# Optimization experiments

Measured on AMD Instinct MI355X. Metric: run time of the kernel, lower is better.

The kernel has to match this reference:

```python
import jax, jax.numpy as jnp
import numpy as np

N_NODES = 100000
N_EDGES = 1600000
HIDDEN_DIM = 64
EIGS_DIM = 32


def setup_inputs() -> dict:
    key = jax.random.key(0)
    k1, k2, k3, k4, k5 = jax.random.split(key, 5)
    q = jax.random.normal(k1, (N_NODES, HIDDEN_DIM), dtype=jnp.float32)
    k = jax.random.normal(k2, (N_NODES, HIDDEN_DIM), dtype=jnp.float32)
    v = jax.random.normal(k3, (N_NODES, HIDDEN_DIM), dtype=jnp.float32)
    eigs = jax.random.normal(k4, (N_NODES, EIGS_DIM), dtype=jnp.float32)
    lambda0 = jnp.zeros((1,), dtype=jnp.float32)  # nn.Parameter(torch.zeros(1))
    indices = jax.random.randint(k5, (2, N_EDGES), 0, N_NODES, dtype=jnp.int64)
    return {"q": q, "k": k, "v": v, "eigs": eigs, "lambda0": lambda0,
            "indices": indices}


def reference(q, k, v, eigs, lambda0, indices):
    n = q.shape[0]
    inv_sqrt_dim = 1.0 / jnp.sqrt(jnp.asarray(q.shape[1], dtype=q.dtype))
    i0 = indices[0]  # destination/row node per edge
    i1 = indices[1]  # source/col node per edge

    # per-edge attention logits: gather-dot-product
    x = jnp.sum(q[i0] * k[i1], axis=-1) * inv_sqrt_dim          # [E]
    y = jnp.sum(eigs[i0] * eigs[i1], axis=-1)                   # [E]
    s = x + jnp.exp(lambda0[0]) * y                             # [E]

    # sparse softmax: clamp(exp(s), -5, 5) then segment-normalize by row sum
    e = jnp.clip(jnp.exp(s), -5.0, 5.0)                         # [E]
    denom = jax.ops.segment_sum(e, i0, num_segments=n)          # [N]
    denom = jnp.where(denom == 0.0, 1.0, denom)
    w = e / denom[i0]                                           # [E]

    # spmm: out[r] = sum_{edges with row r} w_e * v[col_e]
    out = jax.ops.segment_sum(w[:, None] * v[i1], i0, num_segments=n)  # [N, D]
    return out
```

## Files before the change

kernel.cpp:

```cpp
#include <hip/hip_runtime.h>
#include <hip/hip_fp16.h>


#define HD 64
#define ED 32
#define CAP 64
#define RPP 256
#define PSHIFT 8
#define D1 36
#define NB1 256
#define PCAP 5120
#define SPILL_CAP 131072

struct h4 { __half2 a, b; };

__global__ void cvt16_kernel(const float* __restrict__ src,
                             __half* __restrict__ dst, long long n4) {
    long long t = (long long)blockIdx.x * blockDim.x + threadIdx.x;
    long long stride = (long long)gridDim.x * blockDim.x;
    for (; t < n4; t += stride) {
        float4 f = ((const float4*)src)[t];
        h4 h;
        h.a = __floats2half2_rn(f.x, f.y);
        h.b = __floats2half2_rn(f.z, f.w);
        ((h4*)dst)[t] = h;
    }
}

__global__ void p1_bin_kernel(const int* __restrict__ idx, int n_edges,
                              int NP, int chunk,
                              int* __restrict__ part, int* __restrict__ gcur,
                              long long* __restrict__ spill,
                              int* __restrict__ spill_cnt,
                              int* __restrict__ flag) {
    extern __shared__ int sm[];
    int* cnt   = sm;
    int* sbase = sm + NP;
    int* bins  = sm + 2 * NP;
    int tid = threadIdx.x;

    for (int i = tid; i < NP; i += 256) cnt[i] = 0;
    __syncthreads();

    int e0 = blockIdx.x * chunk;
    int n  = n_edges - e0; if (n > chunk) n = chunk; if (n < 0) n = 0;

    for (int i = tid; i < n; i += 256) {
        int e = e0 + i;
        int r = idx[e];
        int c = idx[n_edges + e];
        int p = r >> PSHIFT;
        int w = ((r & (RPP - 1)) << 17) | c;
        int pos = atomicAdd(&cnt[p], 1);
        if (pos < D1) {
            bins[p * D1 + pos] = w;
        } else {
            int s = atomicAdd(spill_cnt, 1);
            if (s < SPILL_CAP) spill[s] = ((long long)r << 32) | (unsigned)c;
            else *flag = 1;
        }
    }
    __syncthreads();

    for (int p = tid; p < NP; p += 256) {
        int m = cnt[p]; if (m > D1) m = D1;
        sbase[p] = (m > 0) ? atomicAdd(&gcur[p], m) : 0;
    }
    __syncthreads();

    int wave = tid >> 6;
    int lane = tid & 63;
    for (int p = wave; p < NP; p += 4) {
        int m = cnt[p]; if (m > D1) m = D1;
        if (lane < m) {
            int slot = sbase[p] + lane;
            int w = bins[p * D1 + lane];
            if (slot < PCAP) {
                part[p * PCAP + slot] = w;
            } else {
                int r = (p << PSHIFT) | (w >> 17);
                int c = w & 0x1FFFF;
                int s = atomicAdd(spill_cnt, 1);
                if (s < SPILL_CAP) spill[s] = ((long long)r << 32) | (unsigned)c;
                else *flag = 1;
            }
        }
    }
}

__global__ void p2_bucket_kernel(const int* __restrict__ part,
                                 const int* __restrict__ gcur,
                                 int* __restrict__ count,
                                 int* __restrict__ bucket, int n_nodes) {
    __shared__ int cnt[RPP / 2];
    __shared__ int win[(RPP / 2) * CAP];
    int tid = threadIdx.x;
    if (tid < RPP / 2) cnt[tid] = 0;
    __syncthreads();

    int p    = blockIdx.x >> 1;
    int half = blockIdx.x & 1;
    int n = gcur[p]; if (n > PCAP) n = PCAP;

    for (int i = tid; i < n; i += 256) {
        int w  = part[p * PCAP + i];
        int rl = w >> 17;
        if ((rl >> 7) != half) continue;
        int rh = rl & 127;
        int c  = w & 0x1FFFF;
        int pos = atomicAdd(&cnt[rh], 1);
        if (pos < CAP) win[(rh << 6) + pos] = c;
    }
    __syncthreads();

    int r0 = (p << PSHIFT) + (half << 7);
    int rows = n_nodes - r0;
    if (rows > RPP / 2) rows = RPP / 2;
    if (rows > 0) {
        int nint4 = rows * (CAP / 4);
        int4* dst = (int4*)(bucket + (long long)r0 * CAP);
        const int4* src = (const int4*)win;
        for (int i = tid; i < nint4; i += 256) dst[i] = src[i];
        if (tid < rows) count[r0 + tid] = cnt[tid];
    }
}

__global__ void spill_drain_kernel(const long long* __restrict__ spill,
                                   const int* __restrict__ spill_cnt,
                                   int* __restrict__ count,
                                   int* __restrict__ bucket) {
    int ns = *spill_cnt; if (ns > SPILL_CAP) ns = SPILL_CAP;
    int stride = gridDim.x * blockDim.x;
    for (int t = blockIdx.x * blockDim.x + threadIdx.x; t < ns; t += stride) {
        long long wc = spill[t];
        int r = (int)(wc >> 32);
        int c = (int)(wc & 0xFFFFFFFFLL);
        int pos = atomicAdd(&count[r], 1);
        if (pos < CAP) bucket[(long long)r * CAP + pos] = c;
    }
}

__global__ void repair_zero_kernel(const int* __restrict__ flag,
                                   int* __restrict__ count, int n_nodes) {
    if (*flag == 0) return;
    int t = blockIdx.x * blockDim.x + threadIdx.x;
    if (t < n_nodes) count[t] = 0;
}

__global__ void repair_scatter_kernel(const int* __restrict__ flag,
                                      const int* __restrict__ idx,
                                      int* __restrict__ count,
                                      int* __restrict__ bucket, int n_edges) {
    if (*flag == 0) return;
    int t = blockIdx.x * blockDim.x + threadIdx.x;
    if (t < n_edges) {
        int r = idx[t];
        int c = idx[n_edges + t];
        int p = atomicAdd(&count[r], 1);
        if (p < CAP) bucket[(long long)r * CAP + p] = c;
    }
}

__global__ void bucket_scatter_kernel(const int* __restrict__ idx,
                                      int* __restrict__ count,
                                      int* __restrict__ bucket, int n_edges) {
    int t = blockIdx.x * blockDim.x + threadIdx.x;
    if (t < n_edges) {
        int r = idx[t];
        int c = idx[n_edges + t];
        int p = atomicAdd(&count[r], 1);
        if (p < CAP) bucket[(long long)r * CAP + p] = c;
    }
}

__global__ void row16_kernel(const float* __restrict__ q,
                             const __half* __restrict__ k16,
                             const __half* __restrict__ v16,
                             const float* __restrict__ eigs,
                             const __half* __restrict__ e16,
                             const float* __restrict__ lambda0,
                             const int* __restrict__ counts,
                             const int* __restrict__ col,
                             const float* __restrict__ kf,
                             const float* __restrict__ vf,
                             const int* __restrict__ idx, int n_edges,
                             float* __restrict__ out, int n_nodes) {
    long long tid = (long long)blockIdx.x * blockDim.x + threadIdx.x;
    int r = (int)(tid >> 6);
    if (r >= n_nodes) return;
    int lane = threadIdx.x & 63;
    int sub = lane & 15;
    int grp = lane >> 4;

    int deg = counts[r];
    const float expL = __expf(lambda0[0]);

    if (deg > CAP) {
        float qs = q[(long long)r * HD + lane] * 0.125f;
        float gs = (lane < ED) ? eigs[(long long)r * ED + lane] * expL : 0.f;
        float accs = 0.f, den = 0.f;
        for (int base = 0; base < n_edges; base += 64) {
            int e = base + lane;
            int rr = (e < n_edges) ? idx[e] : -1;
            int cc = (e < n_edges) ? idx[n_edges + e] : 0;
            unsigned long long mm = __ballot(rr == r);
            while (mm) {
                int b = __ffsll(mm) - 1;
                mm &= mm - 1;
                int c = __shfl(cc, b, 64);
                float kb = kf[(long long)c * HD + lane];
                float gb = (lane < ED) ? eigs[(long long)c * ED + lane] : 0.f;
                float s = qs * kb + gs * gb;
                #pragma unroll
                for (int off = 32; off > 0; off >>= 1) s += __shfl_xor(s, off, 64);
                float e1 = fminf(__expf(s), 5.0f);
                den += e1;
                accs += e1 * vf[(long long)c * HD + lane];
            }
        }
        float inv = (den == 0.f) ? 1.f : __frcp_rn(den);
        out[(long long)r * HD + lane] = accs * inv;
        return;
    }

    long long start = (long long)r * CAP;

    float4 qa = *(const float4*)(q    + (long long)r * HD + sub * 4);
    float2 ga = *(const float2*)(eigs + (long long)r * ED + sub * 2);
    qa.x *= 0.125f; qa.y *= 0.125f; qa.z *= 0.125f; qa.w *= 0.125f;
    ga.x *= expL;   ga.y *= expL;

    float4 acc = make_float4(0.f, 0.f, 0.f, 0.f);
    float den = 0.f;

    for (int base = 0; base < deg; base += 64) {
        int m = deg - base; if (m > 64) m = 64;
        int cl = (lane < m) ? col[start + base + lane] : 0;
        for (int j = 0; j < m; j += 16) {
            int c1 = __shfl(cl, j + grp,      64);
            int c2 = __shfl(cl, j + 4 + grp,  64);
            int c3 = __shfl(cl, j + 8 + grp,  64);
            int c4 = __shfl(cl, j + 12 + grp, 64);
            h4 kb1 = *(const h4*)(k16 + (long long)c1 * HD + sub * 4);
            __half2 gh1 = *(const __half2*)(e16 + (long long)c1 * ED + sub * 2);
            h4 vv1 = *(const h4*)(v16 + (long long)c1 * HD + sub * 4);
            h4 kb2 = *(const h4*)(k16 + (long long)c2 * HD + sub * 4);
            __half2 gh2 = *(const __half2*)(e16 + (long long)c2 * ED + sub * 2);
            h4 vv2 = *(const h4*)(v16 + (long long)c2 * HD + sub * 4);
            h4 kb3 = *(const h4*)(k16 + (long long)c3 * HD + sub * 4);
            __half2 gh3 = *(const __half2*)(e16 + (long long)c3 * ED + sub * 2);
            h4 vv3 = *(const h4*)(v16 + (long long)c3 * HD + sub * 4);
            h4 kb4 = *(const h4*)(k16 + (long long)c4 * HD + sub * 4);
            __half2 gh4 = *(const __half2*)(e16 + (long long)c4 * ED + sub * 2);
            h4 vv4 = *(const h4*)(v16 + (long long)c4 * HD + sub * 4);

            float s1 = qa.x*__low2float(kb1.a) + qa.y*__high2float(kb1.a)
                     + qa.z*__low2float(kb1.b) + qa.w*__high2float(kb1.b)
                     + ga.x*__low2float(gh1)   + ga.y*__high2float(gh1);
            float s2 = qa.x*__low2float(kb2.a) + qa.y*__high2float(kb2.a)
                     + qa.z*__low2float(kb2.b) + qa.w*__high2float(kb2.b)
                     + ga.x*__low2float(gh2)   + ga.y*__high2float(gh2);
            float s3 = qa.x*__low2float(kb3.a) + qa.y*__high2float(kb3.a)
                     + qa.z*__low2float(kb3.b) + qa.w*__high2float(kb3.b)
                     + ga.x*__low2float(gh3)   + ga.y*__high2float(gh3);
            float s4 = qa.x*__low2float(kb4.a) + qa.y*__high2float(kb4.a)
                     + qa.z*__low2float(kb4.b) + qa.w*__high2float(kb4.b)
                     + ga.x*__low2float(gh4)   + ga.y*__high2float(gh4);
            #pragma unroll
            for (int off = 8; off > 0; off >>= 1) {
                s1 += __shfl_xor(s1, off, 64);
                s2 += __shfl_xor(s2, off, 64);
                s3 += __shfl_xor(s3, off, 64);
                s4 += __shfl_xor(s4, off, 64);
            }
            float e1 = fminf(__expf(s1), 5.0f);
            float e2 = fminf(__expf(s2), 5.0f);
            float e3 = fminf(__expf(s3), 5.0f);
            float e4 = fminf(__expf(s4), 5.0f);

            if (j + grp < m) {
                den += e1;
                acc.x += e1 * __low2float(vv1.a); acc.y += e1 * __high2float(vv1.a);
                acc.z += e1 * __low2float(vv1.b); acc.w += e1 * __high2float(vv1.b);
            }
            if (j + 4 + grp < m) {
                den += e2;
                acc.x += e2 * __low2float(vv2.a); acc.y += e2 * __high2float(vv2.a);
                acc.z += e2 * __low2float(vv2.b); acc.w += e2 * __high2float(vv2.b);
            }
            if (j + 8 + grp < m) {
                den += e3;
                acc.x += e3 * __low2float(vv3.a); acc.y += e3 * __high2float(vv3.a);
                acc.z += e3 * __low2float(vv3.b); acc.w += e3 * __high2float(vv3.b);
            }
            if (j + 12 + grp < m) {
                den += e4;
                acc.x += e4 * __low2float(vv4.a); acc.y += e4 * __high2float(vv4.a);
                acc.z += e4 * __low2float(vv4.b); acc.w += e4 * __high2float(vv4.b);
            }
        }
    }

    #pragma unroll
    for (int off = 16; off < 64; off <<= 1) {
        acc.x += __shfl_xor(acc.x, off, 64);
        acc.y += __shfl_xor(acc.y, off, 64);
        acc.z += __shfl_xor(acc.z, off, 64);
        acc.w += __shfl_xor(acc.w, off, 64);
        den   += __shfl_xor(den,   off, 64);
    }

    if (grp == 0) {
        float inv = (den == 0.0f) ? 1.0f : __frcp_rn(den);
        float4 o = make_float4(acc.x * inv, acc.y * inv, acc.z * inv, acc.w * inv);
        *(float4*)(out + (long long)r * HD + sub * 4) = o;
    }
}

__global__ void row_kernel(const float* __restrict__ q, const float* __restrict__ k,
                           const float* __restrict__ v, const float* __restrict__ eigs,
                           const float* __restrict__ lambda0,
                           const int* __restrict__ counts,
                           const int* __restrict__ col,
                           const int* __restrict__ idx, int n_edges,
                           float* __restrict__ out, int n_nodes) {
    long long tid = (long long)blockIdx.x * blockDim.x + threadIdx.x;
    int r = (int)(tid >> 6);
    if (r >= n_nodes) return;
    int lane = threadIdx.x & 63;
    int sub = lane & 15;
    int grp = lane >> 4;

    int deg = counts[r];
    const float expL = __expf(lambda0[0]);

    if (deg > CAP) {
        float qs = q[(long long)r * HD + lane] * 0.125f;
        float gs = (lane < ED) ? eigs[(long long)r * ED + lane] * expL : 0.f;
        float accs = 0.f, den = 0.f;
        for (int base = 0; base < n_edges; base += 64) {
            int e = base + lane;
            int rr = (e < n_edges) ? idx[e] : -1;
            int cc = (e < n_edges) ? idx[n_edges + e] : 0;
            unsigned long long mm = __ballot(rr == r);
            while (mm) {
                int b = __ffsll(mm) - 1;
                mm &= mm - 1;
                int c = __shfl(cc, b, 64);
                float kb = k[(long long)c * HD + lane];
                float gb = (lane < ED) ? eigs[(long long)c * ED + lane] : 0.f;
                float s = qs * kb + gs * gb;
                #pragma unroll
                for (int off = 32; off > 0; off >>= 1) s += __shfl_xor(s, off, 64);
                float e1 = fminf(__expf(s), 5.0f);
                den += e1;
                accs += e1 * v[(long long)c * HD + lane];
            }
        }
        float inv = (den == 0.f) ? 1.f : __frcp_rn(den);
        out[(long long)r * HD + lane] = accs * inv;
        return;
    }

    long long start = (long long)r * CAP;

    float4 qa = *(const float4*)(q    + (long long)r * HD + sub * 4);
    float2 ga = *(const float2*)(eigs + (long long)r * ED + sub * 2);
    qa.x *= 0.125f; qa.y *= 0.125f; qa.z *= 0.125f; qa.w *= 0.125f;
    ga.x *= expL;   ga.y *= expL;

    float4 acc = make_float4(0.f, 0.f, 0.f, 0.f);
    float den = 0.f;

    for (int base = 0; base < deg; base += 64) {
        int m = deg - base; if (m > 64) m = 64;
        int cl = (lane < m) ? col[start + base + lane] : 0;
        for (int j = 0; j < m; j += 8) {
            int c1 = __shfl(cl, j + grp,     64);
            int c2 = __shfl(cl, j + 4 + grp, 64);
            float4 kb1 = *(const float4*)(k    + (long long)c1 * HD + sub * 4);
            float2 gb1 = *(const float2*)(eigs + (long long)c1 * ED + sub * 2);
            float4 vv1 = *(const float4*)(v    + (long long)c1 * HD + sub * 4);
            float4 kb2 = *(const float4*)(k    + (long long)c2 * HD + sub * 4);
            float2 gb2 = *(const float2*)(eigs + (long long)c2 * ED + sub * 2);
            float4 vv2 = *(const float4*)(v    + (long long)c2 * HD + sub * 4);

            float s1 = qa.x*kb1.x + qa.y*kb1.y + qa.z*kb1.z + qa.w*kb1.w
                     + ga.x*gb1.x + ga.y*gb1.y;
            float s2 = qa.x*kb2.x + qa.y*kb2.y + qa.z*kb2.z + qa.w*kb2.w
                     + ga.x*gb2.x + ga.y*gb2.y;
            #pragma unroll
            for (int off = 8; off > 0; off >>= 1) {
                s1 += __shfl_xor(s1, off, 64);
                s2 += __shfl_xor(s2, off, 64);
            }
            float e1 = fminf(__expf(s1), 5.0f);
            float e2 = fminf(__expf(s2), 5.0f);

            if (j + grp < m) {
                den += e1;
                acc.x += e1 * vv1.x; acc.y += e1 * vv1.y;
                acc.z += e1 * vv1.z; acc.w += e1 * vv1.w;
            }
            if (j + 4 + grp < m) {
                den += e2;
                acc.x += e2 * vv2.x; acc.y += e2 * vv2.y;
                acc.z += e2 * vv2.z; acc.w += e2 * vv2.w;
            }
        }
    }

    #pragma unroll
    for (int off = 16; off < 64; off <<= 1) {
        acc.x += __shfl_xor(acc.x, off, 64);
        acc.y += __shfl_xor(acc.y, off, 64);
        acc.z += __shfl_xor(acc.z, off, 64);
        acc.w += __shfl_xor(acc.w, off, 64);
        den   += __shfl_xor(den,   off, 64);
    }

    if (grp == 0) {
        float inv = (den == 0.0f) ? 1.0f : __frcp_rn(den);
        float4 o = make_float4(acc.x * inv, acc.y * inv, acc.z * inv, acc.w * inv);
        *(float4*)(out + (long long)r * HD + sub * 4) = o;
    }
}

__global__ void edge_fused_kernel(const float* __restrict__ q,
                                  const float* __restrict__ k,
                                  const float* __restrict__ v,
                                  const float* __restrict__ eigs,
                                  const float* __restrict__ lambda0,
                                  const int* __restrict__ idx,
                                  float* __restrict__ denom,
                                  float* __restrict__ out, int n_edges) {
    long long gid = (long long)blockIdx.x * blockDim.x + threadIdx.x;
    int lane = threadIdx.x & 63;
    int edge = (int)(gid >> 4);
    int sub  = (int)(gid & 15);
    int valid = (edge < n_edges);
    int ec = valid ? edge : (n_edges - 1);
    int i0 = idx[ec];
    int i1 = idx[n_edges + ec];
    const float expL = __expf(lambda0[0]);
    float4 qa = *(const float4*)(q + (long long)i0 * HD + sub * 4);
    float4 kb = *(const float4*)(k + (long long)i1 * HD + sub * 4);
    float c = (qa.x*kb.x + qa.y*kb.y + qa.z*kb.z + qa.w*kb.w) * 0.125f;
    float2 ea = *(const float2*)(eigs + (long long)i0 * ED + sub * 2);
    float2 eb = *(const float2*)(eigs + (long long)i1 * ED + sub * 2);
    c += expL * (ea.x * eb.x + ea.y * eb.y);
    #pragma unroll
    for (int off = 8; off > 0; off >>= 1) c += __shfl_xor(c, off, 64);
    float e = fminf(__expf(c), 5.0f);
    if (valid && sub == 0) atomicAdd(&denom[i0], e);
    #pragma unroll
    for (int j = 0; j < 4; ++j) {
        float ej = __shfl(e,     j * 16, 64);
        int   r  = __shfl(i0,    j * 16, 64);
        int   s  = __shfl(i1,    j * 16, 64);
        int   vj = __shfl(valid, j * 16, 64);
        if (vj) {
            float vv = v[(long long)s * HD + lane];
            atomicAdd(&out[(long long)r * HD + lane], ej * vv);
        }
    }
}

__global__ void normalize_kernel(float* __restrict__ out,
                                 const float* __restrict__ denom, int n_nodes) {
    int t = blockIdx.x * blockDim.x + threadIdx.x;
    int total = n_nodes * (HD / 4);
    if (t >= total) return;
    int row = t >> 4;
    float d = denom[row];
    float inv = (d == 0.0f) ? 1.0f : __frcp_rn(d);
    float4* o4 = (float4*)out;
    float4 x = o4[t];
    x.x *= inv; x.y *= inv; x.z *= inv; x.w *= inv;
    o4[t] = x;
}

extern "C" void kernel_launch(void* const* d_in, const int* in_sizes, int n_in,
                              void* d_out, int out_size, void* d_ws, size_t ws_size,
                              hipStream_t stream) {
    const float* q       = (const float*)d_in[0];
    const float* k       = (const float*)d_in[1];
    const float* v       = (const float*)d_in[2];
    const float* eigs    = (const float*)d_in[3];
    const float* lambda0 = (const float*)d_in[4];
    const int*   idx     = (const int*)d_in[5];

    const int n_edges = in_sizes[5] / 2;
    const int n_nodes = in_sizes[0] / HD;

    const int NP = (n_nodes + RPP - 1) / RPP;
    const int eb = (n_edges + 255) / 256;
    long long rthreads = (long long)n_nodes * 64;
    const int rb = (int)((rthreads + 255) / 256);

    size_t ints1 = ((size_t)n_nodes + (size_t)n_nodes * CAP
                    + (size_t)NP * PCAP + NP + 2) * sizeof(int);
    size_t need1  = ints1 + 8 + (size_t)SPILL_CAP * sizeof(long long);
    size_t h16    = (size_t)n_nodes * (HD + HD + ED) * sizeof(__half);
    size_t need16 = h16 + need1;
    size_t need2  = ((size_t)n_nodes + (size_t)n_nodes * CAP) * sizeof(int);

    if (ws_size >= need16) {
        char* base = (char*)d_ws;
        __half* k16 = (__half*)base;
        __half* v16 = k16 + (size_t)n_nodes * HD;
        __half* e16 = v16 + (size_t)n_nodes * HD;
        int* count     = (int*)(e16 + (size_t)n_nodes * ED);
        int* bucket    = count + n_nodes;
        int* part      = bucket + (size_t)n_nodes * CAP;
        int* gcur      = part + (size_t)NP * PCAP;
        int* spill_cnt = gcur + NP;
        int* flag      = spill_cnt + 1;
        size_t soff = (size_t)((char*)(flag + 1) - base);
        soff = (soff + 7) & ~(size_t)7;
        long long* spill = (long long*)(base + soff);

        hipMemsetAsync(gcur, 0, (size_t)(NP + 2) * sizeof(int), stream);

        cvt16_kernel<<<1024, 256, 0, stream>>>(k, k16, (long long)n_nodes * HD / 4);
        cvt16_kernel<<<1024, 256, 0, stream>>>(v, v16, (long long)n_nodes * HD / 4);
        cvt16_kernel<<<1024, 256, 0, stream>>>(eigs, e16, (long long)n_nodes * ED / 4);

        int chunk = (n_edges + NB1 - 1) / NB1;
        size_t smbytes = (size_t)NP * (2 + D1) * sizeof(int);
        p1_bin_kernel<<<NB1, 256, smbytes, stream>>>(idx, n_edges, NP, chunk,
                                                     part, gcur, spill,
                                                     spill_cnt, flag);
        p2_bucket_kernel<<<2 * NP, 256, 0, stream>>>(part, gcur, count, bucket,
                                                     n_nodes);
        spill_drain_kernel<<<256, 256, 0, stream>>>(spill, spill_cnt, count,
                                                    bucket);
        repair_zero_kernel<<<(n_nodes + 255) / 256, 256, 0, stream>>>(flag, count,
                                                                      n_nodes);
        repair_scatter_kernel<<<eb, 256, 0, stream>>>(flag, idx, count, bucket,
                                                      n_edges);
        row16_kernel<<<rb, 256, 0, stream>>>(q, k16, v16, eigs, e16, lambda0,
                                             count, bucket, k, v, idx, n_edges,
                                             (float*)d_out, n_nodes);
    } else if (ws_size >= need1) {
        char* base = (char*)d_ws;
        int* count     = (int*)base;
        int* bucket    = count + n_nodes;
        int* part      = bucket + (size_t)n_nodes * CAP;
        int* gcur      = part + (size_t)NP * PCAP;
        int* spill_cnt = gcur + NP;
        int* flag      = spill_cnt + 1;
        size_t soff = (size_t)((char*)(flag + 1) - base);
        soff = (soff + 7) & ~(size_t)7;
        long long* spill = (long long*)(base + soff);

        hipMemsetAsync(gcur, 0, (size_t)(NP + 2) * sizeof(int), stream);

        int chunk = (n_edges + NB1 - 1) / NB1;
        size_t smbytes = (size_t)NP * (2 + D1) * sizeof(int);
        p1_bin_kernel<<<NB1, 256, smbytes, stream>>>(idx, n_edges, NP, chunk,
                                                     part, gcur, spill,
                                                     spill_cnt, flag);
        p2_bucket_kernel<<<2 * NP, 256, 0, stream>>>(part, gcur, count, bucket,
                                                     n_nodes);
        spill_drain_kernel<<<256, 256, 0, stream>>>(spill, spill_cnt, count,
                                                    bucket);
        repair_zero_kernel<<<(n_nodes + 255) / 256, 256, 0, stream>>>(flag, count,
                                                                      n_nodes);
        repair_scatter_kernel<<<eb, 256, 0, stream>>>(flag, idx, count, bucket,
                                                      n_edges);
        row_kernel<<<rb, 256, 0, stream>>>(q, k, v, eigs, lambda0, count, bucket,
                                           idx, n_edges, (float*)d_out, n_nodes);
    } else if (ws_size >= need2) {
        int* count  = (int*)d_ws;
        int* bucket = count + n_nodes;
        hipMemsetAsync(count, 0, (size_t)n_nodes * sizeof(int), stream);
        bucket_scatter_kernel<<<eb, 256, 0, stream>>>(idx, count, bucket, n_edges);
        row_kernel<<<rb, 256, 0, stream>>>(q, k, v, eigs, lambda0, count, bucket,
                                           idx, n_edges, (float*)d_out, n_nodes);
    } else {
        float* denom = (float*)d_ws;
        hipMemsetAsync(denom, 0, (size_t)n_nodes * sizeof(float), stream);
        hipMemsetAsync(d_out, 0, (size_t)out_size * sizeof(float), stream);
        long long threads = (long long)n_edges * 16;
        int grid = (int)((threads + 255) / 256);
        edge_fused_kernel<<<grid, 256, 0, stream>>>(q, k, v, eigs, lambda0, idx,
                                                    denom, (float*)d_out, n_edges);
        int n4 = n_nodes * (HD / 4);
        normalize_kernel<<<(n4 + 255) / 256, 256, 0, stream>>>((float*)d_out,
                                                               denom, n_nodes);
    }
}
```

Baseline: 276.3 us.

## Fuse fp16 conversion into binning kernel, merge spill/repair kernels, retune binning

The three separate fp32-to-fp16 conversion launches are folded into the tail of the edge-binning kernel, and the spill-drain and repair-zero kernels are merged into one launch. The binning kernel now runs 1024 blocks with a smaller per-partition shared bin depth of 16, and its flush loop handles four partitions per wave using 16-lane subgroups. This cuts launch count and raises parallelism in binning. The smaller bins push more edges onto the global spill path, so more atomics may hit the spill counter.

```diff
diff --git a/kernel.cpp b/kernel.cpp
--- a/kernel.cpp
+++ b/kernel.cpp
@@ -7,32 +7,26 @@
 #define CAP 64
 #define RPP 256
 #define PSHIFT 8
-#define D1 36
-#define NB1 256
+#define D1 16
+#define NB1 1024
 #define PCAP 5120
 #define SPILL_CAP 131072
 
 struct h4 { __half2 a, b; };
-
-__global__ void cvt16_kernel(const float* __restrict__ src,
-                             __half* __restrict__ dst, long long n4) {
-    long long t = (long long)blockIdx.x * blockDim.x + threadIdx.x;
-    long long stride = (long long)gridDim.x * blockDim.x;
-    for (; t < n4; t += stride) {
-        float4 f = ((const float4*)src)[t];
-        h4 h;
-        h.a = __floats2half2_rn(f.x, f.y);
-        h.b = __floats2half2_rn(f.z, f.w);
-        ((h4*)dst)[t] = h;
-    }
-}
 
 __global__ void p1_bin_kernel(const int* __restrict__ idx, int n_edges,
                               int NP, int chunk,
                               int* __restrict__ part, int* __restrict__ gcur,
                               long long* __restrict__ spill,
                               int* __restrict__ spill_cnt,
-                              int* __restrict__ flag) {
+                              int* __restrict__ flag,
+                              const float* __restrict__ kf,
+                              const float* __restrict__ vf,
+                              const float* __restrict__ ef,
+                              __half* __restrict__ k16,
+                              __half* __restrict__ v16,
+                              __half* __restrict__ e16,
+                              long long nk4, long long ne4) {
     extern __shared__ int sm[];
     int* cnt   = sm;
     int* sbase = sm + NP;
@@ -70,20 +64,51 @@
 
     int wave = tid >> 6;
     int lane = tid & 63;
-    for (int p = wave; p < NP; p += 4) {
-        int m = cnt[p]; if (m > D1) m = D1;
-        if (lane < m) {
-            int slot = sbase[p] + lane;
-            int w = bins[p * D1 + lane];
-            if (slot < PCAP) {
-                part[p * PCAP + slot] = w;
-            } else {
-                int r = (p << PSHIFT) | (w >> 17);
-                int c = w & 0x1FFFF;
-                int s = atomicAdd(spill_cnt, 1);
-                if (s < SPILL_CAP) spill[s] = ((long long)r << 32) | (unsigned)c;
-                else *flag = 1;
-            }
+    int sg = lane >> 4;
+    int sl = lane & 15;
+    for (int p0 = wave * 4; p0 < NP; p0 += 16) {
+        int p = p0 + sg;
+        if (p < NP) {
+            int m = cnt[p]; if (m > D1) m = D1;
+            if (sl < m) {
+                int slot = sbase[p] + sl;
+                int w = bins[p * D1 + sl];
+                if (slot < PCAP) {
+                    part[p * PCAP + slot] = w;
+                } else {
+                    int r = (p << PSHIFT) | (w >> 17);
+                    int c = w & 0x1FFFF;
+                    int s = atomicAdd(spill_cnt, 1);
+                    if (s < SPILL_CAP) spill[s] = ((long long)r << 32) | (unsigned)c;
+                    else *flag = 1;
+                }
+            }
+        }
+    }
+
+    if (k16 != nullptr) {
+        long long gt = (long long)blockIdx.x * 256 + tid;
+        long long gs = (long long)gridDim.x * 256;
+        for (long long t = gt; t < nk4; t += gs) {
+            float4 f = ((const float4*)kf)[t];
+            h4 h;
+            h.a = __floats2half2_rn(f.x, f.y);
+            h.b = __floats2half2_rn(f.z, f.w);
+            ((h4*)k16)[t] = h;
+        }
+        for (long long t = gt; t < nk4; t += gs) {
+            float4 f = ((const float4*)vf)[t];
+            h4 h;
+            h.a = __floats2half2_rn(f.x, f.y);
+            h.b = __floats2half2_rn(f.z, f.w);
+            ((h4*)v16)[t] = h;
+        }
+        for (long long t = gt; t < ne4; t += gs) {
+            float4 f = ((const float4*)ef)[t];
+            h4 h;
+            h.a = __floats2half2_rn(f.x, f.y);
+            h.b = __floats2half2_rn(f.z, f.w);
+            ((h4*)e16)[t] = h;
         }
     }
 }
@@ -125,26 +150,25 @@
     }
 }
 
-__global__ void spill_drain_kernel(const long long* __restrict__ spill,
-                                   const int* __restrict__ spill_cnt,
-                                   int* __restrict__ count,
-                                   int* __restrict__ bucket) {
+__global__ void spill_or_zero_kernel(const long long* __restrict__ spill,
+                                     const int* __restrict__ spill_cnt,
+                                     const int* __restrict__ flag,
+                                     int* __restrict__ count,
+                                     int* __restrict__ bucket, int n_nodes) {
+    int stride = gridDim.x * blockDim.x;
+    int t0 = blockIdx.x * blockDim.x + threadIdx.x;
+    if (*flag) {
+        for (int t = t0; t < n_nodes; t += stride) count[t] = 0;
+        return;
+    }
     int ns = *spill_cnt; if (ns > SPILL_CAP) ns = SPILL_CAP;
-    int stride = gridDim.x * blockDim.x;
-    for (int t = blockIdx.x * blockDim.x + threadIdx.x; t < ns; t += stride) {
+    for (int t = t0; t < ns; t += stride) {
         long long wc = spill[t];
         int r = (int)(wc >> 32);
         int c = (int)(wc & 0xFFFFFFFFLL);
         int pos = atomicAdd(&count[r], 1);
         if (pos < CAP) bucket[(long long)r * CAP + pos] = c;
     }
-}
-
-__global__ void repair_zero_kernel(const int* __restrict__ flag,
-                                   int* __restrict__ count, int n_nodes) {
-    if (*flag == 0) return;
-    int t = blockIdx.x * blockDim.x + threadIdx.x;
-    if (t < n_nodes) count[t] = 0;
 }
 
 __global__ void repair_scatter_kernel(const int* __restrict__ flag,
@@ -522,21 +546,16 @@
 
         hipMemsetAsync(gcur, 0, (size_t)(NP + 2) * sizeof(int), stream);
 
-        cvt16_kernel<<<1024, 256, 0, stream>>>(k, k16, (long long)n_nodes * HD / 4);
-        cvt16_kernel<<<1024, 256, 0, stream>>>(v, v16, (long long)n_nodes * HD / 4);
-        cvt16_kernel<<<1024, 256, 0, stream>>>(eigs, e16, (long long)n_nodes * ED / 4);
-
         int chunk = (n_edges + NB1 - 1) / NB1;
         size_t smbytes = (size_t)NP * (2 + D1) * sizeof(int);
-        p1_bin_kernel<<<NB1, 256, smbytes, stream>>>(idx, n_edges, NP, chunk,
-                                                     part, gcur, spill,
-                                                     spill_cnt, flag);
+        p1_bin_kernel<<<NB1, 256, smbytes, stream>>>(
+            idx, n_edges, NP, chunk, part, gcur, spill, spill_cnt, flag,
+            k, v, eigs, k16, v16, e16,
+            (long long)n_nodes * HD / 4, (long long)n_nodes * ED / 4);
         p2_bucket_kernel<<<2 * NP, 256, 0, stream>>>(part, gcur, count, bucket,
                                                      n_nodes);
-        spill_drain_kernel<<<256, 256, 0, stream>>>(spill, spill_cnt, count,
-                                                    bucket);
-        repair_zero_kernel<<<(n_nodes + 255) / 256, 256, 0, stream>>>(flag, count,
-                                                                      n_nodes);
+        spill_or_zero_kernel<<<(n_nodes + 255) / 256, 256, 0, stream>>>(
+            spill, spill_cnt, flag, count, bucket, n_nodes);
         repair_scatter_kernel<<<eb, 256, 0, stream>>>(flag, idx, count, bucket,
                                                       n_edges);
         row16_kernel<<<rb, 256, 0, stream>>>(q, k16, v16, eigs, e16, lambda0,
@@ -558,15 +577,13 @@
 
         int chunk = (n_edges + NB1 - 1) / NB1;
         size_t smbytes = (size_t)NP * (2 + D1) * sizeof(int);
-        p1_bin_kernel<<<NB1, 256, smbytes, stream>>>(idx, n_edges, NP, chunk,
-                                                     part, gcur, spill,
-                                                     spill_cnt, flag);
+        p1_bin_kernel<<<NB1, 256, smbytes, stream>>>(
+            idx, n_edges, NP, chunk, part, gcur, spill, spill_cnt, flag,
+            nullptr, nullptr, nullptr, nullptr, nullptr, nullptr, 0, 0);
         p2_bucket_kernel<<<2 * NP, 256, 0, stream>>>(part, gcur, count, bucket,
                                                      n_nodes);
-        spill_drain_kernel<<<256, 256, 0, stream>>>(spill, spill_cnt, count,
-                                                    bucket);
-        repair_zero_kernel<<<(n_nodes + 255) / 256, 256, 0, stream>>>(flag, count,
-                                                                      n_nodes);
+        spill_or_zero_kernel<<<(n_nodes + 255) / 256, 256, 0, stream>>>(
+            spill, spill_cnt, flag, count, bucket, n_nodes);
         repair_scatter_kernel<<<eb, 256, 0, stream>>>(flag, idx, count, bucket,
                                                       n_edges);
         row_kernel<<<rb, 256, 0, stream>>>(q, k, v, eigs, lambda0, count, bucket,
```

New measurement: 263.4 us. 1.05x faster.
